# Kernel tuning notes

Measured on AMD Instinct MI355X. Metric: run time of the kernel, lower is better.

The kernel has to match this reference:

```python
import jax, jax.numpy as jnp
import numpy as np

B = 4096
D = 256
TEMP = 0.5


def setup_inputs() -> dict:
    key = jax.random.key(0)
    k1, k2 = jax.random.split(key)
    x_i = jax.random.normal(k1, (B, D), dtype=jnp.float32)
    x_j = jax.random.normal(k2, (B, D), dtype=jnp.float32)
    return {"x_i": x_i, "x_j": x_j}


def reference(x_i, x_j):
    b = x_i.shape[0]
    # L2-normalize rows (F.normalize with default eps=1e-12)
    def l2norm(x):
        n = jnp.linalg.norm(x, axis=1, keepdims=True)
        return x / jnp.maximum(n, 1e-12)

    z = jnp.concatenate([l2norm(x_i), l2norm(x_j)], axis=0)  # [2B, D]
    # rows of z are unit-norm, so cosine similarity == dot product
    sim = z @ z.T  # [2B, 2B]

    # positives: diagonals at offsets +B and -B
    idx = jnp.arange(b)
    sim_ij = sim[idx, idx + b]
    sim_ji = sim[idx + b, idx]
    pos = jnp.concatenate([sim_ij, sim_ji], axis=0)  # [2B]

    nom = jnp.exp(pos / TEMP)
    neg_mask = 1.0 - jnp.eye(2 * b, dtype=sim.dtype)
    denom = jnp.sum(neg_mask * jnp.exp(sim / TEMP), axis=1)  # [2B]
    loss = jnp.sum(-jnp.log(nom / denom)) / (2 * b)
    return loss
```

## Files before the change

kernel.cpp:

```cpp
#include <hip/hip_runtime.h>

#define NB   4096
#define ND   256
#define N2B  8192
#define INV_T 2.0f

typedef __attribute__((ext_vector_type(8))) short bf16x8;
typedef __attribute__((ext_vector_type(4))) float f32x4;

__device__ __forceinline__ void gload_lds16(const void* g, void* l) {
  __builtin_amdgcn_global_load_lds(
      (const __attribute__((address_space(1))) void*)g,
      (__attribute__((address_space(3))) void*)l, 16, 0, 0);
}

__device__ __forceinline__ unsigned short f2b(float f) {
  unsigned int u = __float_as_uint(f);
  u = (u + 0x7fffu + ((u >> 16) & 1u)) >> 16;
  return (unsigned short)u;
}
__device__ __forceinline__ float b2f(unsigned short h) {
  return __uint_as_float(((unsigned int)h) << 16);
}

__global__ __launch_bounds__(256) void k_normalize(
    const float* __restrict__ xi, const float* __restrict__ xj,
    unsigned short* __restrict__ Z, float* __restrict__ diagE,
    float* __restrict__ pos, float* __restrict__ lossAcc,
    unsigned int* __restrict__ ticket) {
  __shared__ float sh[2][256];
  if (blockIdx.x == 0 && threadIdx.x == 0) { *lossAcc = 0.0f; *ticket = 0u; }
  int wave = threadIdx.x >> 6, lane = threadIdx.x & 63;
  int r = (int)blockIdx.x * 2 + (wave & 1);
  bool isJ = wave >= 2;
  const float* src = (isJ ? xj : xi) + (size_t)r * ND;
  int zrow = r + (isJ ? NB : 0);

  float4 v = *(const float4*)(src + lane * 4);
  float ss = v.x * v.x + v.y * v.y + v.z * v.z + v.w * v.w;
#pragma unroll
  for (int m = 1; m < 64; m <<= 1) ss += __shfl_xor(ss, m, 64);
  float scale = 1.0f / fmaxf(sqrtf(ss), 1e-12f);
  unsigned short h0 = f2b(v.x * scale), h1 = f2b(v.y * scale);
  unsigned short h2 = f2b(v.z * scale), h3 = f2b(v.w * scale);
  ushort4 st; st.x = h0; st.y = h1; st.z = h2; st.w = h3;
  *(ushort4*)(Z + (size_t)zrow * ND + lane * 4) = st;

  float f0 = b2f(h0), f1 = b2f(h1), f2 = b2f(h2), f3 = b2f(h3);
  float d = f0 * f0 + f1 * f1 + f2 * f2 + f3 * f3;
#pragma unroll
  for (int m = 1; m < 64; m <<= 1) d += __shfl_xor(d, m, 64);
  if (lane == 0) diagE[zrow] = __expf(d * INV_T);

  if (isJ) {
    float* s = sh[wave & 1] + lane * 4;
    s[0] = f0; s[1] = f1; s[2] = f2; s[3] = f3;
  }
  __syncthreads();
  if (!isJ) {
    const float* s = sh[wave] + lane * 4;
    float p = f0 * s[0] + f1 * s[1] + f2 * s[2] + f3 * s[3];
#pragma unroll
    for (int m = 1; m < 64; m <<= 1) p += __shfl_xor(p, m, 64);
    if (lane == 0) pos[r] = p;
  }
}

#define CT 64
__global__ __launch_bounds__(256) void k_gemm_exp(
    const unsigned short* __restrict__ Z, float* __restrict__ R) {
  __shared__ alignas(16) unsigned short Bs[CT * ND];

  int tid = threadIdx.x;
  int wave = tid >> 6, lane = tid & 63;
  int band = (int)blockIdx.x >> 3;
  int colq = (int)blockIdx.x & 7;
  int quad = lane >> 4, c16 = lane & 15;

  bf16x8 afr[2][8];
  int rowA = band * 128 + wave * 32;
#pragma unroll
  for (int rg = 0; rg < 2; ++rg)
#pragma unroll
    for (int kk = 0; kk < 8; ++kk)
      afr[rg][kk] = *(const bf16x8*)(Z + (size_t)(rowA + rg * 16 + c16) * ND +
                                     kk * 32 + quad * 8);

  float rs[2][4];
#pragma unroll
  for (int rg = 0; rg < 2; ++rg)
#pragma unroll
    for (int r = 0; r < 4; ++r) rs[rg][r] = 0.0f;

  int lr1 = lane >> 5;
  int cs = lane & 31;

  for (int ct = 0; ct < 16; ++ct) {
    int colbase = colq * 1024 + ct * CT;
    __syncthreads();
#pragma unroll
    for (int j = 0; j < 8; ++j) {
      int r0 = wave * 16 + j * 2;
      int row = r0 + lr1;
      int gc = cs ^ (row & 31);
      gload_lds16(Z + (size_t)(colbase + row) * ND + gc * 8, &Bs[r0 * ND]);
    }
    asm volatile("s_waitcnt vmcnt(0)" ::: "memory");
    __syncthreads();

    f32x4 acc[2][4] = {};
#pragma unroll
    for (int kk = 0; kk < 8; ++kk) {
      bf16x8 bfr[4];
#pragma unroll
      for (int ni = 0; ni < 4; ++ni) {
        int row = ni * 16 + c16;
        int slot = (kk * 4 + quad) ^ (row & 31);
        bfr[ni] = *(const bf16x8*)&Bs[row * ND + slot * 8];
      }
#pragma unroll
      for (int rg = 0; rg < 2; ++rg)
#pragma unroll
        for (int ni = 0; ni < 4; ++ni)
          acc[rg][ni] = __builtin_amdgcn_mfma_f32_16x16x32_bf16(
              afr[rg][kk], bfr[ni], acc[rg][ni], 0, 0, 0);
    }

#pragma unroll
    for (int rg = 0; rg < 2; ++rg)
#pragma unroll
      for (int ni = 0; ni < 4; ++ni)
#pragma unroll
        for (int r = 0; r < 4; ++r)
          rs[rg][r] += __expf(acc[rg][ni][r] * INV_T);
  }

#pragma unroll
  for (int m = 1; m <= 8; m <<= 1)
#pragma unroll
    for (int rg = 0; rg < 2; ++rg)
#pragma unroll
      for (int r = 0; r < 4; ++r)
        rs[rg][r] += __shfl_xor(rs[rg][r], m, 64);

#pragma unroll
  for (int rg = 0; rg < 2; ++rg)
#pragma unroll
    for (int r = 0; r < 4; ++r)
      if (c16 == rg * 4 + r) {
        int row = rowA + rg * 16 + quad * 4 + r;
        R[(size_t)row * 8 + colq] = rs[rg][r];
      }
}

__global__ __launch_bounds__(256) void k_final(
    const float* __restrict__ R, const float* __restrict__ diagE,
    const float* __restrict__ pos, float* __restrict__ lossAcc,
    unsigned int* __restrict__ ticket, float* __restrict__ out) {
  __shared__ float red[4];
  int tid = threadIdx.x;
  int wave = tid >> 6, lane = tid & 63;
  int row = (int)blockIdx.x * 256 + tid;

  const float* Rr = R + (size_t)row * 8;
  float4 a = *(const float4*)(Rr);
  float4 b = *(const float4*)(Rr + 4);
  float s = (a.x + a.y + a.z + a.w) + (b.x + b.y + b.z + b.w) - diagE[row];
  float term = __logf(s) - INV_T * pos[row & (NB - 1)];
#pragma unroll
  for (int m = 1; m < 64; m <<= 1) term += __shfl_xor(term, m, 64);
  if (lane == 0) red[wave] = term;
  __syncthreads();
  if (tid == 0) {
    float bs = red[0] + red[1] + red[2] + red[3];
    atomicAdd(lossAcc, bs);
    __threadfence();
    unsigned int old = atomicAdd(ticket, 1u);
    if (old == 31u) {
      float v = atomicAdd(lossAcc, 0.0f);
      out[0] = v * (1.0f / (float)N2B);
    }
  }
}

extern "C" void kernel_launch(void* const* d_in, const int* in_sizes, int n_in,
                              void* d_out, int out_size, void* d_ws,
                              size_t ws_size, hipStream_t stream) {
  const float* xi = (const float*)d_in[0];
  const float* xj = (const float*)d_in[1];
  float* out = (float*)d_out;
  char* ws = (char*)d_ws;
  unsigned short* Z = (unsigned short*)ws;
  float* R = (float*)(ws + (4u << 20));
  float* pos = (float*)(ws + (8u << 20));
  float* diagE = (float*)(ws + (8u << 20) + 65536);
  float* lossAcc = (float*)(ws + (8u << 20) + 131072);
  unsigned int* ticket = (unsigned int*)(ws + (8u << 20) + 131072 + 64);

  k_normalize<<<dim3(NB / 2), dim3(256), 0, stream>>>(xi, xj, Z, diagE, pos,
                                                      lossAcc, ticket);
  k_gemm_exp<<<dim3(512), dim3(256), 0, stream>>>(Z, R);
  k_final<<<dim3(32), dim3(256), 0, stream>>>(R, diagE, pos, lossAcc, ticket,
                                              out);
}
```

Measured before the change: 100.2 us.

## Use 32x32 MFMA with larger row tiles and double-buffered LDS staging

Switches the GEMM+exp kernel from 16x16x32 to 32x32x16 bf16 MFMA. Each wave now holds 64 A rows in registers, and each block covers 256 rows by 512 columns, which gives 16 column spans and a wider R buffer. B tiles are double-buffered in LDS, with the next tile prefetched while the current one is computed, so global-load latency overlaps with MFMA/exp work. The larger register footprint (A fragments plus 32 accumulators per lane) may limit occupancy; the launch bound requests 2 blocks.

```diff
diff --git a/kernel.cpp b/kernel.cpp
--- a/kernel.cpp
+++ b/kernel.cpp
@@ -6,7 +6,7 @@
 #define INV_T 2.0f
 
 typedef __attribute__((ext_vector_type(8))) short bf16x8;
-typedef __attribute__((ext_vector_type(4))) float f32x4;
+typedef __attribute__((ext_vector_type(16))) float f32x16;
 
 __device__ __forceinline__ void gload_lds16(const void* g, void* l) {
   __builtin_amdgcn_global_load_lds(
@@ -66,91 +66,95 @@
   }
 }
 
-#define CT 64
-__global__ __launch_bounds__(256) void k_gemm_exp(
+__global__ __launch_bounds__(256, 2) void k_gemm_exp(
     const unsigned short* __restrict__ Z, float* __restrict__ R) {
-  __shared__ alignas(16) unsigned short Bs[CT * ND];
+  __shared__ alignas(16) unsigned short Bs[2][64 * ND];
 
   int tid = threadIdx.x;
   int wave = tid >> 6, lane = tid & 63;
-  int band = (int)blockIdx.x >> 3;
-  int colq = (int)blockIdx.x & 7;
-  int quad = lane >> 4, c16 = lane & 15;
-
-  bf16x8 afr[2][8];
-  int rowA = band * 128 + wave * 32;
+  int r5 = lane & 31, h = lane >> 5;
+  int band = (int)blockIdx.x >> 4;
+  int span = (int)blockIdx.x & 15;
+  int rowA = band * 256 + wave * 64;
+  int colspan = span * 512;
+
+  bf16x8 afr[2][16];
 #pragma unroll
   for (int rg = 0; rg < 2; ++rg)
 #pragma unroll
-    for (int kk = 0; kk < 8; ++kk)
-      afr[rg][kk] = *(const bf16x8*)(Z + (size_t)(rowA + rg * 16 + c16) * ND +
-                                     kk * 32 + quad * 8);
-
-  float rs[2][4];
+    for (int kk = 0; kk < 16; ++kk)
+      afr[rg][kk] = *(const bf16x8*)(Z + (size_t)(rowA + rg * 32 + r5) * ND +
+                                     kk * 16 + h * 8);
+
+  float rs[2][16];
 #pragma unroll
   for (int rg = 0; rg < 2; ++rg)
 #pragma unroll
-    for (int r = 0; r < 4; ++r) rs[rg][r] = 0.0f;
-
-  int lr1 = lane >> 5;
-  int cs = lane & 31;
-
-  for (int ct = 0; ct < 16; ++ct) {
-    int colbase = colq * 1024 + ct * CT;
+    for (int g = 0; g < 16; ++g) rs[rg][g] = 0.0f;
+
+#define STAGE(t, b)                                                         \
+  {                                                                         \
+    int colbase = colspan + (t)*64;                                         \
+    _Pragma("unroll") for (int call = 0; call < 8; ++call) {                \
+      int r0 = wave * 16 + call * 2;                                        \
+      int zr = colbase + r0 + h;                                            \
+      int gc = r5 ^ (zr & 31);                                              \
+      gload_lds16(Z + (size_t)zr * ND + gc * 8, &Bs[b][r0 * ND]);           \
+    }                                                                       \
+  }
+
+  STAGE(0, 0)
+  STAGE(1, 1)
+
+#pragma unroll
+  for (int t = 0; t < 8; ++t) {
+    if (t < 7)
+      asm volatile("s_waitcnt vmcnt(8)" ::: "memory");
+    else
+      asm volatile("s_waitcnt vmcnt(0)" ::: "memory");
     __syncthreads();
-#pragma unroll
-    for (int j = 0; j < 8; ++j) {
-      int r0 = wave * 16 + j * 2;
-      int row = r0 + lr1;
-      int gc = cs ^ (row & 31);
-      gload_lds16(Z + (size_t)(colbase + row) * ND + gc * 8, &Bs[r0 * ND]);
+
+    const unsigned short* Bb = &Bs[t & 1][0];
+#pragma unroll
+    for (int ni = 0; ni < 2; ++ni) {
+      f32x16 acc0 = {};
+      f32x16 acc1 = {};
+#pragma unroll
+      for (int kk = 0; kk < 16; ++kk) {
+        bf16x8 bf =
+            *(const bf16x8*)&Bb[(ni * 32 + r5) * ND + (((kk * 2 + h) ^ r5) * 8)];
+        acc0 = __builtin_amdgcn_mfma_f32_32x32x16_bf16(afr[0][kk], bf, acc0, 0,
+                                                       0, 0);
+        acc1 = __builtin_amdgcn_mfma_f32_32x32x16_bf16(afr[1][kk], bf, acc1, 0,
+                                                       0, 0);
+      }
+#pragma unroll
+      for (int g = 0; g < 16; ++g) {
+        rs[0][g] += __expf(acc0[g] * INV_T);
+        rs[1][g] += __expf(acc1[g] * INV_T);
+      }
     }
-    asm volatile("s_waitcnt vmcnt(0)" ::: "memory");
     __syncthreads();
-
-    f32x4 acc[2][4] = {};
-#pragma unroll
-    for (int kk = 0; kk < 8; ++kk) {
-      bf16x8 bfr[4];
-#pragma unroll
-      for (int ni = 0; ni < 4; ++ni) {
-        int row = ni * 16 + c16;
-        int slot = (kk * 4 + quad) ^ (row & 31);
-        bfr[ni] = *(const bf16x8*)&Bs[row * ND + slot * 8];
+    if (t + 2 < 8) STAGE(t + 2, t & 1)
+  }
+
+#pragma unroll
+  for (int m = 1; m <= 16; m <<= 1)
+#pragma unroll
+    for (int rg = 0; rg < 2; ++rg)
+#pragma unroll
+      for (int g = 0; g < 16; ++g)
+        rs[rg][g] += __shfl_xor(rs[rg][g], m, 64);
+
+#pragma unroll
+  for (int rg = 0; rg < 2; ++rg)
+#pragma unroll
+    for (int g = 0; g < 16; ++g)
+      if (r5 == g) {
+        int rowIn = (g & 3) + 8 * (g >> 2) + 4 * h;
+        R[(size_t)(rowA + rg * 32 + rowIn) * 16 + span] = rs[rg][g];
       }
-#pragma unroll
-      for (int rg = 0; rg < 2; ++rg)
-#pragma unroll
-        for (int ni = 0; ni < 4; ++ni)
-          acc[rg][ni] = __builtin_amdgcn_mfma_f32_16x16x32_bf16(
-              afr[rg][kk], bfr[ni], acc[rg][ni], 0, 0, 0);
-    }
-
-#pragma unroll
-    for (int rg = 0; rg < 2; ++rg)
-#pragma unroll
-      for (int ni = 0; ni < 4; ++ni)
-#pragma unroll
-        for (int r = 0; r < 4; ++r)
-          rs[rg][r] += __expf(acc[rg][ni][r] * INV_T);
-  }
-
-#pragma unroll
-  for (int m = 1; m <= 8; m <<= 1)
-#pragma unroll
-    for (int rg = 0; rg < 2; ++rg)
-#pragma unroll
-      for (int r = 0; r < 4; ++r)
-        rs[rg][r] += __shfl_xor(rs[rg][r], m, 64);
-
-#pragma unroll
-  for (int rg = 0; rg < 2; ++rg)
-#pragma unroll
-    for (int r = 0; r < 4; ++r)
-      if (c16 == rg * 4 + r) {
-        int row = rowA + rg * 16 + quad * 4 + r;
-        R[(size_t)row * 8 + colq] = rs[rg][r];
-      }
+#undef STAGE
 }
 
 __global__ __launch_bounds__(256) void k_final(
@@ -162,10 +166,13 @@
   int wave = tid >> 6, lane = tid & 63;
   int row = (int)blockIdx.x * 256 + tid;
 
-  const float* Rr = R + (size_t)row * 8;
-  float4 a = *(const float4*)(Rr);
-  float4 b = *(const float4*)(Rr + 4);
-  float s = (a.x + a.y + a.z + a.w) + (b.x + b.y + b.z + b.w) - diagE[row];
+  const float* Rr = R + (size_t)row * 16;
+  float s = -diagE[row];
+#pragma unroll
+  for (int i = 0; i < 4; ++i) {
+    float4 a = *(const float4*)(Rr + i * 4);
+    s += (a.x + a.y) + (a.z + a.w);
+  }
   float term = __logf(s) - INV_T * pos[row & (NB - 1)];
 #pragma unroll
   for (int m = 1; m < 64; m <<= 1) term += __shfl_xor(term, m, 64);
```

New measurement: 105.8 us. 5.6% more time.

## Double-buffer B tiles in LDS and fold exp scale into prescaled A operand

Applied to the files above, without the earlier changes.

The GEMM+exp kernel now double-buffers the B column tiles in LDS, issuing async global->LDS loads two tiles ahead and waiting with partial vmcnt so loads overlap the MFMA work. The A operand comes from a second bf16 copy of Z prescaled by 2/ln2, which turns the exponential into a bare exp2f and drops one multiply per element. Launch bounds ask for two blocks per CU. The trade-offs are double the LDS use, an extra 4MB workspace write in the normalize kernel, and one more bf16 rounding step on the prescaled operand.

```diff
diff --git a/kernel.cpp b/kernel.cpp
--- a/kernel.cpp
+++ b/kernel.cpp
@@ -4,6 +4,7 @@
 #define ND   256
 #define N2B  8192
 #define INV_T 2.0f
+#define C_EXP 2.8853900817779268f
 
 typedef __attribute__((ext_vector_type(8))) short bf16x8;
 typedef __attribute__((ext_vector_type(4))) float f32x4;
@@ -25,9 +26,9 @@
 
 __global__ __launch_bounds__(256) void k_normalize(
     const float* __restrict__ xi, const float* __restrict__ xj,
-    unsigned short* __restrict__ Z, float* __restrict__ diagE,
-    float* __restrict__ pos, float* __restrict__ lossAcc,
-    unsigned int* __restrict__ ticket) {
+    unsigned short* __restrict__ Z, unsigned short* __restrict__ Zs,
+    float* __restrict__ diagE, float* __restrict__ pos,
+    float* __restrict__ lossAcc, unsigned int* __restrict__ ticket) {
   __shared__ float sh[2][256];
   if (blockIdx.x == 0 && threadIdx.x == 0) { *lossAcc = 0.0f; *ticket = 0u; }
   int wave = threadIdx.x >> 6, lane = threadIdx.x & 63;
@@ -47,6 +48,11 @@
   *(ushort4*)(Z + (size_t)zrow * ND + lane * 4) = st;
 
   float f0 = b2f(h0), f1 = b2f(h1), f2 = b2f(h2), f3 = b2f(h3);
+  ushort4 sts;
+  sts.x = f2b(f0 * C_EXP); sts.y = f2b(f1 * C_EXP);
+  sts.z = f2b(f2 * C_EXP); sts.w = f2b(f3 * C_EXP);
+  *(ushort4*)(Zs + (size_t)zrow * ND + lane * 4) = sts;
+
   float d = f0 * f0 + f1 * f1 + f2 * f2 + f3 * f3;
 #pragma unroll
   for (int m = 1; m < 64; m <<= 1) d += __shfl_xor(d, m, 64);
@@ -67,9 +73,10 @@
 }
 
 #define CT 64
-__global__ __launch_bounds__(256) void k_gemm_exp(
-    const unsigned short* __restrict__ Z, float* __restrict__ R) {
-  __shared__ alignas(16) unsigned short Bs[CT * ND];
+__global__ __launch_bounds__(256, 2) void k_gemm_exp(
+    const unsigned short* __restrict__ Zs, const unsigned short* __restrict__ Z,
+    float* __restrict__ R) {
+  __shared__ alignas(16) unsigned short Bs[2][CT * ND];
 
   int tid = threadIdx.x;
   int wave = tid >> 6, lane = tid & 63;
@@ -83,7 +90,7 @@
   for (int rg = 0; rg < 2; ++rg)
 #pragma unroll
     for (int kk = 0; kk < 8; ++kk)
-      afr[rg][kk] = *(const bf16x8*)(Z + (size_t)(rowA + rg * 16 + c16) * ND +
+      afr[rg][kk] = *(const bf16x8*)(Zs + (size_t)(rowA + rg * 16 + c16) * ND +
                                      kk * 32 + quad * 8);
 
   float rs[2][4];
@@ -95,19 +102,30 @@
   int lr1 = lane >> 5;
   int cs = lane & 31;
 
-  for (int ct = 0; ct < 16; ++ct) {
-    int colbase = colq * 1024 + ct * CT;
-    __syncthreads();
-#pragma unroll
-    for (int j = 0; j < 8; ++j) {
-      int r0 = wave * 16 + j * 2;
-      int row = r0 + lr1;
-      int gc = cs ^ (row & 31);
-      gload_lds16(Z + (size_t)(colbase + row) * ND + gc * 8, &Bs[r0 * ND]);
-    }
-    asm volatile("s_waitcnt vmcnt(0)" ::: "memory");
-    __syncthreads();
-
+#define STAGE(t, b)                                                       \
+  {                                                                       \
+    int colbase = colq * 1024 + (t)*CT;                                   \
+    _Pragma("unroll") for (int call = 0; call < 8; ++call) {              \
+      int r0 = wave * 16 + call * 2;                                      \
+      int row = r0 + lr1;                                                 \
+      int gc = cs ^ (row & 31);                                           \
+      gload_lds16(Z + (size_t)(colbase + row) * ND + gc * 8,              \
+                  &Bs[b][r0 * ND]);                                       \
+    }                                                                     \
+  }
+
+  STAGE(0, 0)
+  STAGE(1, 1)
+
+#pragma unroll 2
+  for (int t = 0; t < 16; ++t) {
+    if (t == 15)
+      asm volatile("s_waitcnt vmcnt(0)" ::: "memory");
+    else
+      asm volatile("s_waitcnt vmcnt(8)" ::: "memory");
+    __builtin_amdgcn_s_barrier();
+
+    const unsigned short* Bb = &Bs[t & 1][0];
     f32x4 acc[2][4] = {};
 #pragma unroll
     for (int kk = 0; kk < 8; ++kk) {
@@ -116,7 +134,7 @@
       for (int ni = 0; ni < 4; ++ni) {
         int row = ni * 16 + c16;
         int slot = (kk * 4 + quad) ^ (row & 31);
-        bfr[ni] = *(const bf16x8*)&Bs[row * ND + slot * 8];
+        bfr[ni] = *(const bf16x8*)&Bb[row * ND + slot * 8];
       }
 #pragma unroll
       for (int rg = 0; rg < 2; ++rg)
@@ -132,8 +150,13 @@
       for (int ni = 0; ni < 4; ++ni)
 #pragma unroll
         for (int r = 0; r < 4; ++r)
-          rs[rg][r] += __expf(acc[rg][ni][r] * INV_T);
-  }
+          rs[rg][r] += exp2f(acc[rg][ni][r]);
+
+    asm volatile("s_waitcnt lgkmcnt(0)" ::: "memory");
+    __builtin_amdgcn_s_barrier();
+    if (t + 2 < 16) STAGE(t + 2, t & 1)
+  }
+#undef STAGE
 
 #pragma unroll
   for (int m = 1; m <= 8; m <<= 1)
@@ -191,15 +214,16 @@
   float* out = (float*)d_out;
   char* ws = (char*)d_ws;
   unsigned short* Z = (unsigned short*)ws;
-  float* R = (float*)(ws + (4u << 20));
-  float* pos = (float*)(ws + (8u << 20));
-  float* diagE = (float*)(ws + (8u << 20) + 65536);
-  float* lossAcc = (float*)(ws + (8u << 20) + 131072);
-  unsigned int* ticket = (unsigned int*)(ws + (8u << 20) + 131072 + 64);
-
-  k_normalize<<<dim3(NB / 2), dim3(256), 0, stream>>>(xi, xj, Z, diagE, pos,
-                                                      lossAcc, ticket);
-  k_gemm_exp<<<dim3(512), dim3(256), 0, stream>>>(Z, R);
+  unsigned short* Zs = (unsigned short*)(ws + (4u << 20));
+  float* R = (float*)(ws + (8u << 20));
+  float* pos = (float*)(ws + (9u << 20));
+  float* diagE = (float*)(ws + (9u << 20) + 65536);
+  float* lossAcc = (float*)(ws + (9u << 20) + 131072);
+  unsigned int* ticket = (unsigned int*)(ws + (9u << 20) + 131072 + 64);
+
+  k_normalize<<<dim3(NB / 2), dim3(256), 0, stream>>>(xi, xj, Z, Zs, diagE,
+                                                      pos, lossAcc, ticket);
+  k_gemm_exp<<<dim3(512), dim3(256), 0, stream>>>(Zs, Z, R);
   k_final<<<dim3(32), dim3(256), 0, stream>>>(R, diagE, pos, lossAcc, ticket,
                                               out);
 }
```

Result: slower. 108.8 us (+8.6%).
